# Kernel optimization log

Measured on AMD Instinct MI355X. Metric: run time of the kernel, lower is better.

The kernel has to match this reference:

```python
import jax, jax.numpy as jnp
import numpy as np

N_NODES = 50000
N_EDGES = 600000
FEAT = 128
N_LAYERS = 4


def setup_inputs() -> dict:
    key = jax.random.key(0)
    ks = jax.random.split(key, 7)
    feats = jax.random.normal(ks[0], (N_NODES, FEAT), dtype=jnp.float32)
    src = jax.random.randint(ks[1], (N_EDGES,), 0, N_NODES)
    dst = jax.random.randint(ks[2], (N_EDGES,), 0, N_NODES)
    s = 1.0 / np.sqrt(FEAT)  # torch Linear default init range
    theta_w = jax.random.uniform(ks[3], (N_LAYERS, FEAT, FEAT), jnp.float32, -s, s)
    theta_b = jax.random.uniform(ks[4], (N_LAYERS, FEAT), jnp.float32, -s, s)
    phi_w = jax.random.uniform(ks[5], (N_LAYERS, FEAT, FEAT), jnp.float32, -s, s)
    phi_b = jax.random.uniform(ks[6], (N_LAYERS, FEAT), jnp.float32, -s, s)
    return {"feats": feats, "src": src, "dst": dst,
            "theta_w": theta_w, "theta_b": theta_b,
            "phi_w": phi_w, "phi_b": phi_b}


def _edgeconv(x, src, dst, tw, tb, pw, pb):
    # EdgeConv (Wang et al. 2018): out_i = max_{(j->i) in E} theta(x_j - x_i) + phi(x_i)
    phi = x @ pw.T + pb                       # [N, F] node-level linear (avoid per-edge recompute)
    diff = x[src] - x[dst]                    # [E, F] gather
    msg = diff @ tw.T + tb + phi[dst]         # [E, F]
    agg = jax.ops.segment_max(msg, dst, num_segments=x.shape[0])  # [N, F]
    # nodes with no incoming edges get -inf from segment_max; zero them (DGL convention)
    return jnp.where(jnp.isneginf(agg), jnp.zeros_like(agg), agg)


def reference(feats, src, dst, theta_w, theta_b, phi_w, phi_b):
    x = feats
    for l in range(N_LAYERS):
        x = _edgeconv(x, src, dst, theta_w[l], theta_b[l], phi_w[l], phi_b[l])
        x = jax.nn.relu(x)
    return x
```

## Files before the change

kernel.cpp:

```cpp
#include <hip/hip_runtime.h>

#define FEAT 128

typedef __attribute__((ext_vector_type(8))) _Float16 f16x8;
typedef __attribute__((ext_vector_type(2))) _Float16 f16x2;
typedef __attribute__((ext_vector_type(4))) float f32x4;

static __device__ __forceinline__ int wave_incl_scan(int v, int lane) {
#pragma unroll
    for (int off = 1; off < 64; off <<= 1) {
        int u = __shfl_up(v, off, 64);
        if (lane >= off) v += u;
    }
    return v;
}


__global__ void hist_kernel(const int* __restrict__ dst, int* __restrict__ deg, int E) {
    int e = blockIdx.x * blockDim.x + threadIdx.x;
    if (e < E) atomicAdd(&deg[dst[e]], 1);
}

__global__ __launch_bounds__(1024) void scan1_kernel(const int* __restrict__ deg,
                                                     int* __restrict__ row_ptr,
                                                     int* __restrict__ bsum, int N) {
    int i = blockIdx.x * 1024 + threadIdx.x;
    int lane = threadIdx.x & 63;
    int w = threadIdx.x >> 6;
    int v = (i < N) ? deg[i] : 0;
    int inc = wave_incl_scan(v, lane);
    __shared__ int wsum[16];
    if (lane == 63) wsum[w] = inc;
    __syncthreads();
    if (w == 0) {
        int s = (lane < 16) ? wsum[lane] : 0;
        int si = wave_incl_scan(s, lane);
        if (lane < 16) wsum[lane] = si - s;
    }
    __syncthreads();
    int exc = inc - v + wsum[w];
    if (i < N) row_ptr[i] = exc;
    if (threadIdx.x == 1023) bsum[blockIdx.x] = exc + v;
}

__global__ __launch_bounds__(1024) void scan2_kernel(const int* __restrict__ bsum,
                                                     int* __restrict__ boff,
                                                     int* __restrict__ row_ptr,
                                                     int nb, int N, int E) {
    int tid = threadIdx.x;
    int lane = tid & 63;
    int w = tid >> 6;
    int v = (tid < nb) ? bsum[tid] : 0;
    int inc = wave_incl_scan(v, lane);
    __shared__ int wsum[16];
    if (lane == 63) wsum[w] = inc;
    __syncthreads();
    if (w == 0) {
        int s = (lane < 16) ? wsum[lane] : 0;
        int si = wave_incl_scan(s, lane);
        if (lane < 16) wsum[lane] = si - s;
    }
    __syncthreads();
    if (tid < nb) boff[tid] = inc - v + wsum[w];
    if (tid == 0) row_ptr[N] = E;
}

__global__ void scan3_kernel(int* __restrict__ row_ptr, const int* __restrict__ boff, int N) {
    int i = blockIdx.x * blockDim.x + threadIdx.x;
    if (i < N) row_ptr[i] += boff[i >> 10];
}


__global__ void wcvt_kernel(const float* __restrict__ tw, const float* __restrict__ pw,
                            const float* __restrict__ tb, const float* __restrict__ pb,
                            _Float16* __restrict__ wt, _Float16* __restrict__ wp,
                            float* __restrict__ bsum, int n, int nbias) {
    int i = blockIdx.x * blockDim.x + threadIdx.x;
    if (i < n) { wt[i] = (_Float16)tw[i]; wp[i] = (_Float16)pw[i]; }
    if (i < nbias) bsum[i] = tb[i] + pb[i];
}

__global__ void xcvt_kernel(const float* __restrict__ x, _Float16* __restrict__ x16, int n4) {
    int i = blockIdx.x * blockDim.x + threadIdx.x;
    if (i < n4) {
        float4 v = ((const float4*)x)[i];
        f16x2 a, b;
        a[0] = (_Float16)v.x; a[1] = (_Float16)v.y;
        b[0] = (_Float16)v.z; b[1] = (_Float16)v.w;
        ((f16x2*)x16)[i * 2] = a;
        ((f16x2*)x16)[i * 2 + 1] = b;
    }
}


static __device__ __forceinline__ void gemm_body(
        int bx,
        const _Float16* __restrict__ x16,
        const _Float16* __restrict__ wt, const _Float16* __restrict__ wp,
        const float* __restrict__ bias,
        _Float16* __restrict__ t16, _Float16* __restrict__ q16, int M) {
    int lane = threadIdx.x & 63;
    int l16 = lane & 15;
    int quad = lane >> 4;
    int cn0 = (threadIdx.x >> 6) * 32;

    f16x8 bt[2][4], bp[2][4];
    float biasv[2];
#pragma unroll
    for (int ct = 0; ct < 2; ++ct) {
        int col = cn0 + ct * 16 + l16;
        biasv[ct] = bias[col];
#pragma unroll
        for (int kk = 0; kk < 4; ++kk) {
            int k = kk * 32 + quad * 8;
            bt[ct][kk] = *(const f16x8*)(wt + (size_t)col * FEAT + k);
            bp[ct][kk] = *(const f16x8*)(wp + (size_t)col * FEAT + k);
        }
    }

    int rbase0 = bx * 128;
#pragma unroll 1
    for (int rs = 0; rs < 8; ++rs) {
        int rbase = rbase0 + rs * 16;
        int row = rbase + l16;
        int rowc = (row < M) ? row : (M - 1);
        f16x8 a[4];
#pragma unroll
        for (int kk = 0; kk < 4; ++kk)
            a[kk] = *(const f16x8*)(x16 + (size_t)rowc * FEAT + kk * 32 + quad * 8);

        f32x4 accT[2] = {{0.f, 0.f, 0.f, 0.f}, {0.f, 0.f, 0.f, 0.f}};
        f32x4 accP[2] = {{0.f, 0.f, 0.f, 0.f}, {0.f, 0.f, 0.f, 0.f}};
#pragma unroll
        for (int kk = 0; kk < 4; ++kk) {
#pragma unroll
            for (int ct = 0; ct < 2; ++ct) {
                accT[ct] = __builtin_amdgcn_mfma_f32_16x16x32_f16(a[kk], bt[ct][kk], accT[ct], 0, 0, 0);
                accP[ct] = __builtin_amdgcn_mfma_f32_16x16x32_f16(a[kk], bp[ct][kk], accP[ct], 0, 0, 0);
            }
        }
#pragma unroll
        for (int ct = 0; ct < 2; ++ct) {
            int col = cn0 + ct * 16 + l16;
#pragma unroll
            for (int r = 0; r < 4; ++r) {
                int ro = rbase + quad * 4 + r;
                if (ro < M) {
                    t16[(size_t)ro * FEAT + col] = (_Float16)accT[ct][r];
                    q16[(size_t)ro * FEAT + col] =
                        (_Float16)(accP[ct][r] - accT[ct][r] + biasv[ct]);
                }
            }
        }
    }
}

__global__ __launch_bounds__(256) void mfma_gemm_kernel(
        const _Float16* __restrict__ x16,
        const _Float16* __restrict__ wt, const _Float16* __restrict__ wp,
        const float* __restrict__ bias,
        _Float16* __restrict__ t16, _Float16* __restrict__ q16, int M) {
    gemm_body(blockIdx.x, x16, wt, wp, bias, t16, q16, M);
}

__global__ __launch_bounds__(256) void fused0_kernel(
        const _Float16* __restrict__ x16,
        const _Float16* __restrict__ wt, const _Float16* __restrict__ wp,
        const float* __restrict__ bias,
        _Float16* __restrict__ t16, _Float16* __restrict__ q16, int M, int gb,
        const int* __restrict__ src, const int* __restrict__ dst,
        const int* __restrict__ row_ptr, int* __restrict__ fill,
        int* __restrict__ esrc, int E) {
    if ((int)blockIdx.x < gb) {
        gemm_body(blockIdx.x, x16, wt, wp, bias, t16, q16, M);
    } else {
        int e = (blockIdx.x - gb) * 256 + threadIdx.x;
        if (e < E) {
            int d = dst[e];
            int pos = row_ptr[d] + atomicAdd(&fill[d], 1);
            esrc[pos] = src[e];
        }
    }
}


static __device__ __forceinline__ f16x8 vmax8(f16x8 a, f16x8 b) {
#pragma unroll
    for (int i = 0; i < 8; ++i) a[i] = (a[i] > b[i]) ? a[i] : b[i];
    return a;
}

static __device__ __forceinline__ f16x8 shflxor8(f16x8 v, int mask) {
    union { f16x8 h; int i[4]; } u;
    u.h = v;
#pragma unroll
    for (int k = 0; k < 4; ++k) u.i[k] = __shfl_xor(u.i[k], mask, 64);
    return u.h;
}

__global__ __launch_bounds__(256) void agg_kernel(
        const _Float16* __restrict__ t16, const _Float16* __restrict__ q16,
        const int* __restrict__ row_ptr, const int* __restrict__ esrc,
        float* __restrict__ outf, _Float16* __restrict__ ox, int N) {
    int wv = threadIdx.x >> 6;
    int lane = threadIdx.x & 63;
    int node = blockIdx.x * 4 + wv;
    if (node >= N) return;

    int g = lane >> 4;
    int c = lane & 15;

    int beg = row_ptr[node];
    int end = row_ptr[node + 1];

    if (beg >= end) {
        if (outf && g == 0) {
            float4 z = make_float4(0.f, 0.f, 0.f, 0.f);
            ((float4*)(outf + (size_t)node * FEAT + c * 8))[0] = z;
            ((float4*)(outf + (size_t)node * FEAT + c * 8))[1] = z;
        }
        if (ox && g == 0) {
            f16x8 z = {};
            *(f16x8*)(ox + (size_t)node * FEAT + c * 8) = z;
        }
        return;
    }

    const _Float16 NEGINF = (_Float16)(-65504.0f);
    f16x8 m0, m1, m2, m3;
#pragma unroll
    for (int i = 0; i < 8; ++i) { m0[i] = NEGINF; m1[i] = NEGINF; m2[i] = NEGINF; m3[i] = NEGINF; }

    for (int base = beg; base < end; base += 64) {
        int n = end - base;
        if (n > 64) n = 64;
        int nm1 = n - 1;
        int li = (lane < n) ? lane : nm1;
        int myidx = esrc[base + li];
        for (int j = 0; j < n; j += 16) {
            bool b1 = (j + 4) < n, b2 = (j + 8) < n, b3 = (j + 12) < n;
            int s0 = j + g;       if (s0 > nm1) s0 = nm1;
            f16x8 v0 = *(const f16x8*)(t16 + (size_t)__shfl(myidx, s0) * FEAT + c * 8);
            f16x8 v1, v2, v3;
            if (b1) {
                int s1 = j + 4 + g;  if (s1 > nm1) s1 = nm1;
                v1 = *(const f16x8*)(t16 + (size_t)__shfl(myidx, s1) * FEAT + c * 8);
            }
            if (b2) {
                int s2 = j + 8 + g;  if (s2 > nm1) s2 = nm1;
                v2 = *(const f16x8*)(t16 + (size_t)__shfl(myidx, s2) * FEAT + c * 8);
            }
            if (b3) {
                int s3 = j + 12 + g; if (s3 > nm1) s3 = nm1;
                v3 = *(const f16x8*)(t16 + (size_t)__shfl(myidx, s3) * FEAT + c * 8);
            }
            m0 = vmax8(m0, v0);
            if (b1) m1 = vmax8(m1, v1);
            if (b2) m2 = vmax8(m2, v2);
            if (b3) m3 = vmax8(m3, v3);
        }
    }

    f16x8 m = vmax8(vmax8(m0, m1), vmax8(m2, m3));

    m = vmax8(m, shflxor8(m, 16));
    m = vmax8(m, shflxor8(m, 32));

    if (g == 0) {
        f16x8 qi = *(const f16x8*)(q16 + (size_t)node * FEAT + c * 8);
        float o[8];
#pragma unroll
        for (int i = 0; i < 8; ++i)
            o[i] = fmaxf((float)m[i] + (float)qi[i], 0.f);

        if (outf) {
            float4 o0 = make_float4(o[0], o[1], o[2], o[3]);
            float4 o1 = make_float4(o[4], o[5], o[6], o[7]);
            ((float4*)(outf + (size_t)node * FEAT + c * 8))[0] = o0;
            ((float4*)(outf + (size_t)node * FEAT + c * 8))[1] = o1;
        }
        if (ox) {
            f16x8 oh;
#pragma unroll
            for (int i = 0; i < 8; ++i) oh[i] = (_Float16)o[i];
            *(f16x8*)(ox + (size_t)node * FEAT + c * 8) = oh;
        }
    }
}


extern "C" void kernel_launch(void* const* d_in, const int* in_sizes, int n_in,
                              void* d_out, int out_size, void* d_ws, size_t ws_size,
                              hipStream_t stream) {
    const float* feats   = (const float*)d_in[0];
    const int*   src     = (const int*)d_in[1];
    const int*   dst     = (const int*)d_in[2];
    const float* theta_w = (const float*)d_in[3];
    const float* theta_b = (const float*)d_in[4];
    const float* phi_w   = (const float*)d_in[5];
    const float* phi_b   = (const float*)d_in[6];

    const int N = in_sizes[0] / FEAT;
    const int E = in_sizes[1];
    const int L = in_sizes[3] / (FEAT * FEAT);

    char* ws = (char*)d_ws;
    size_t off = 0;
    auto alloc = [&](size_t bytes) -> void* {
        void* ptr = ws + off;
        off = (off + bytes + 255) & ~(size_t)255;
        return ptr;
    };
    _Float16* t16 = (_Float16*)alloc((size_t)N * FEAT * 2);
    _Float16* q16 = (_Float16*)alloc((size_t)N * FEAT * 2);
    _Float16* x16 = (_Float16*)alloc((size_t)N * FEAT * 2);
    _Float16* wt16 = (_Float16*)alloc((size_t)L * FEAT * FEAT * 2);
    _Float16* wp16 = (_Float16*)alloc((size_t)L * FEAT * FEAT * 2);
    float* bsum_b = (float*)alloc((size_t)L * FEAT * sizeof(float));
    int* deg     = (int*)alloc((size_t)N * sizeof(int));
    int* fill    = (int*)alloc((size_t)N * sizeof(int));
    int* row_ptr = (int*)alloc((size_t)(N + 1) * sizeof(int));
    int* esrc    = (int*)alloc((size_t)E * sizeof(int));
    int* bsum    = (int*)alloc(2048 * sizeof(int));
    int* boff    = (int*)alloc(2048 * sizeof(int));
    (void)ws_size;

    hipMemsetAsync(deg, 0, (size_t)N * sizeof(int), stream);
    hipMemsetAsync(fill, 0, (size_t)N * sizeof(int), stream);

    int eb = (E + 255) / 256;
    int nb = (N + 1023) >> 10;
    hist_kernel<<<eb, 256, 0, stream>>>(dst, deg, E);
    scan1_kernel<<<nb, 1024, 0, stream>>>(deg, row_ptr, bsum, N);
    scan2_kernel<<<1, 1024, 0, stream>>>(bsum, boff, row_ptr, nb, N, E);
    scan3_kernel<<<(N + 255) / 256, 256, 0, stream>>>(row_ptr, boff, N);

    int wn = L * FEAT * FEAT;
    wcvt_kernel<<<(wn + 255) / 256, 256, 0, stream>>>(
        theta_w, phi_w, theta_b, phi_b, wt16, wp16, bsum_b, wn, L * FEAT);
    int xn4 = N * FEAT / 4;
    xcvt_kernel<<<(xn4 + 255) / 256, 256, 0, stream>>>(feats, x16, xn4);

    int gb = (N + 127) / 128;
    for (int l = 0; l < L; ++l) {
        if (l == 0) {
            fused0_kernel<<<gb + eb, 256, 0, stream>>>(
                x16, wt16, wp16, bsum_b, t16, q16, N, gb,
                src, dst, row_ptr, fill, esrc, E);
        } else {
            mfma_gemm_kernel<<<gb, 256, 0, stream>>>(
                x16,
                wt16 + (size_t)l * FEAT * FEAT,
                wp16 + (size_t)l * FEAT * FEAT,
                bsum_b + (size_t)l * FEAT,
                t16, q16, N);
        }

        bool last = (l == L - 1);
        agg_kernel<<<(N + 3) / 4, 256, 0, stream>>>(
            t16, q16,
            row_ptr, esrc,
            last ? (float*)d_out : nullptr,
            last ? nullptr : x16,
            N);
    }
}
```

Measured before the change: 338.9 us.

## Bucket CSR edges by source slab and fuse preprocessing kernels

Builds the CSR with four sub-buckets per destination node, keyed by which quarter of the node range the source falls in. Edges are therefore gathered slab by slab, so that concurrent waves touch a smaller working set of t16 and cache reuse improves. The histogram, weight conversion and feature conversion kernels are merged into one launch. The GEMM moves to 64 rows per block for more blocks, and the aggregation loop drops the early exit for empty nodes. The cost is a scan four times larger, four row-pointer reads per node, and a single max accumulator chain.

```diff
diff --git a/kernel.cpp b/kernel.cpp
--- a/kernel.cpp
+++ b/kernel.cpp
@@ -1,6 +1,7 @@
 #include <hip/hip_runtime.h>
 
 #define FEAT 128
+#define SLABS 4
 
 typedef __attribute__((ext_vector_type(8))) _Float16 f16x8;
 typedef __attribute__((ext_vector_type(2))) _Float16 f16x2;
@@ -16,18 +17,46 @@
 }
 
 
-__global__ void hist_kernel(const int* __restrict__ dst, int* __restrict__ deg, int E) {
-    int e = blockIdx.x * blockDim.x + threadIdx.x;
-    if (e < E) atomicAdd(&deg[dst[e]], 1);
-}
+__global__ void prep_kernel(const int* __restrict__ src, const int* __restrict__ dst,
+                            int* __restrict__ deg4, int E, int slab_size,
+                            const float* __restrict__ tw, const float* __restrict__ pw,
+                            const float* __restrict__ tb, const float* __restrict__ pb,
+                            _Float16* __restrict__ wt, _Float16* __restrict__ wp,
+                            float* __restrict__ bsum, int wn, int nbias,
+                            const float* __restrict__ x, _Float16* __restrict__ x16, int xn4,
+                            int hb, int wb) {
+    int bid = blockIdx.x;
+    if (bid < hb) {
+        int e = bid * 256 + threadIdx.x;
+        if (e < E) {
+            int sl = src[e] / slab_size;
+            atomicAdd(&deg4[dst[e] * SLABS + sl], 1);
+        }
+    } else if (bid < hb + wb) {
+        int i = (bid - hb) * 256 + threadIdx.x;
+        if (i < wn) { wt[i] = (_Float16)tw[i]; wp[i] = (_Float16)pw[i]; }
+        if (i < nbias) bsum[i] = tb[i] + pb[i];
+    } else {
+        int i = (bid - hb - wb) * 256 + threadIdx.x;
+        if (i < xn4) {
+            float4 v = ((const float4*)x)[i];
+            f16x2 a, b;
+            a[0] = (_Float16)v.x; a[1] = (_Float16)v.y;
+            b[0] = (_Float16)v.z; b[1] = (_Float16)v.w;
+            ((f16x2*)x16)[i * 2] = a;
+            ((f16x2*)x16)[i * 2 + 1] = b;
+        }
+    }
+}
+
 
 __global__ __launch_bounds__(1024) void scan1_kernel(const int* __restrict__ deg,
                                                      int* __restrict__ row_ptr,
-                                                     int* __restrict__ bsum, int N) {
+                                                     int* __restrict__ bsum, int N4) {
     int i = blockIdx.x * 1024 + threadIdx.x;
     int lane = threadIdx.x & 63;
     int w = threadIdx.x >> 6;
-    int v = (i < N) ? deg[i] : 0;
+    int v = (i < N4) ? deg[i] : 0;
     int inc = wave_incl_scan(v, lane);
     __shared__ int wsum[16];
     if (lane == 63) wsum[w] = inc;
@@ -39,14 +68,14 @@
     }
     __syncthreads();
     int exc = inc - v + wsum[w];
-    if (i < N) row_ptr[i] = exc;
+    if (i < N4) row_ptr[i] = exc;
     if (threadIdx.x == 1023) bsum[blockIdx.x] = exc + v;
 }
 
 __global__ __launch_bounds__(1024) void scan2_kernel(const int* __restrict__ bsum,
                                                      int* __restrict__ boff,
                                                      int* __restrict__ row_ptr,
-                                                     int nb, int N, int E) {
+                                                     int nb, int N4, int E) {
     int tid = threadIdx.x;
     int lane = tid & 63;
     int w = tid >> 6;
@@ -62,34 +91,12 @@
     }
     __syncthreads();
     if (tid < nb) boff[tid] = inc - v + wsum[w];
-    if (tid == 0) row_ptr[N] = E;
-}
-
-__global__ void scan3_kernel(int* __restrict__ row_ptr, const int* __restrict__ boff, int N) {
+    if (tid == 0) row_ptr[N4] = E;
+}
+
+__global__ void scan3_kernel(int* __restrict__ row_ptr, const int* __restrict__ boff, int N4) {
     int i = blockIdx.x * blockDim.x + threadIdx.x;
-    if (i < N) row_ptr[i] += boff[i >> 10];
-}
-
-
-__global__ void wcvt_kernel(const float* __restrict__ tw, const float* __restrict__ pw,
-                            const float* __restrict__ tb, const float* __restrict__ pb,
-                            _Float16* __restrict__ wt, _Float16* __restrict__ wp,
-                            float* __restrict__ bsum, int n, int nbias) {
-    int i = blockIdx.x * blockDim.x + threadIdx.x;
-    if (i < n) { wt[i] = (_Float16)tw[i]; wp[i] = (_Float16)pw[i]; }
-    if (i < nbias) bsum[i] = tb[i] + pb[i];
-}
-
-__global__ void xcvt_kernel(const float* __restrict__ x, _Float16* __restrict__ x16, int n4) {
-    int i = blockIdx.x * blockDim.x + threadIdx.x;
-    if (i < n4) {
-        float4 v = ((const float4*)x)[i];
-        f16x2 a, b;
-        a[0] = (_Float16)v.x; a[1] = (_Float16)v.y;
-        b[0] = (_Float16)v.z; b[1] = (_Float16)v.w;
-        ((f16x2*)x16)[i * 2] = a;
-        ((f16x2*)x16)[i * 2 + 1] = b;
-    }
+    if (i < N4) row_ptr[i] += boff[i >> 10];
 }
 
 
@@ -118,9 +125,9 @@
         }
     }
 
-    int rbase0 = bx * 128;
+    int rbase0 = bx * 64;
 #pragma unroll 1
-    for (int rs = 0; rs < 8; ++rs) {
+    for (int rs = 0; rs < 4; ++rs) {
         int rbase = rbase0 + rs * 16;
         int row = rbase + l16;
         int rowc = (row < M) ? row : (M - 1);
@@ -169,16 +176,17 @@
         const float* __restrict__ bias,
         _Float16* __restrict__ t16, _Float16* __restrict__ q16, int M, int gb,
         const int* __restrict__ src, const int* __restrict__ dst,
-        const int* __restrict__ row_ptr, int* __restrict__ fill,
-        int* __restrict__ esrc, int E) {
+        const int* __restrict__ row_ptr4, int* __restrict__ fill4,
+        int* __restrict__ esrc, int E, int slab_size) {
     if ((int)blockIdx.x < gb) {
         gemm_body(blockIdx.x, x16, wt, wp, bias, t16, q16, M);
     } else {
         int e = (blockIdx.x - gb) * 256 + threadIdx.x;
         if (e < E) {
-            int d = dst[e];
-            int pos = row_ptr[d] + atomicAdd(&fill[d], 1);
-            esrc[pos] = src[e];
+            int s = src[e];
+            int key = dst[e] * SLABS + s / slab_size;
+            int pos = row_ptr4[key] + atomicAdd(&fill4[key], 1);
+            esrc[pos] = s;
         }
     }
 }
@@ -200,7 +208,7 @@
 
 __global__ __launch_bounds__(256) void agg_kernel(
         const _Float16* __restrict__ t16, const _Float16* __restrict__ q16,
-        const int* __restrict__ row_ptr, const int* __restrict__ esrc,
+        const int* __restrict__ row_ptr4, const int* __restrict__ esrc,
         float* __restrict__ outf, _Float16* __restrict__ ox, int N) {
     int wv = threadIdx.x >> 6;
     int lane = threadIdx.x & 63;
@@ -210,58 +218,46 @@
     int g = lane >> 4;
     int c = lane & 15;
 
-    int beg = row_ptr[node];
-    int end = row_ptr[node + 1];
-
-    if (beg >= end) {
-        if (outf && g == 0) {
-            float4 z = make_float4(0.f, 0.f, 0.f, 0.f);
-            ((float4*)(outf + (size_t)node * FEAT + c * 8))[0] = z;
-            ((float4*)(outf + (size_t)node * FEAT + c * 8))[1] = z;
-        }
-        if (ox && g == 0) {
-            f16x8 z = {};
-            *(f16x8*)(ox + (size_t)node * FEAT + c * 8) = z;
-        }
-        return;
-    }
-
     const _Float16 NEGINF = (_Float16)(-65504.0f);
-    f16x8 m0, m1, m2, m3;
-#pragma unroll
-    for (int i = 0; i < 8; ++i) { m0[i] = NEGINF; m1[i] = NEGINF; m2[i] = NEGINF; m3[i] = NEGINF; }
-
-    for (int base = beg; base < end; base += 64) {
-        int n = end - base;
-        if (n > 64) n = 64;
-        int nm1 = n - 1;
-        int li = (lane < n) ? lane : nm1;
-        int myidx = esrc[base + li];
-        for (int j = 0; j < n; j += 16) {
-            bool b1 = (j + 4) < n, b2 = (j + 8) < n, b3 = (j + 12) < n;
-            int s0 = j + g;       if (s0 > nm1) s0 = nm1;
-            f16x8 v0 = *(const f16x8*)(t16 + (size_t)__shfl(myidx, s0) * FEAT + c * 8);
-            f16x8 v1, v2, v3;
-            if (b1) {
-                int s1 = j + 4 + g;  if (s1 > nm1) s1 = nm1;
-                v1 = *(const f16x8*)(t16 + (size_t)__shfl(myidx, s1) * FEAT + c * 8);
+    f16x8 m;
+#pragma unroll
+    for (int i = 0; i < 8; ++i) m[i] = NEGINF;
+
+#pragma unroll 1
+    for (int s = 0; s < SLABS; ++s) {
+        int beg = row_ptr4[4 * node + s];
+        int end = row_ptr4[4 * node + s + 1];
+        for (int base = beg; base < end; base += 64) {
+            int n = end - base;
+            if (n > 64) n = 64;
+            int nm1 = n - 1;
+            int li = (lane < n) ? lane : nm1;
+            int myidx = esrc[base + li];
+            for (int j = 0; j < n; j += 16) {
+                bool b1 = (j + 4) < n, b2 = (j + 8) < n, b3 = (j + 12) < n;
+                int s0 = j + g;       if (s0 > nm1) s0 = nm1;
+                f16x8 v0 = *(const f16x8*)(t16 + (size_t)__shfl(myidx, s0) * FEAT + c * 8);
+                f16x8 v1, v2, v3;
+                if (b1) {
+                    int s1 = j + 4 + g;  if (s1 > nm1) s1 = nm1;
+                    v1 = *(const f16x8*)(t16 + (size_t)__shfl(myidx, s1) * FEAT + c * 8);
+                }
+                if (b2) {
+                    int s2 = j + 8 + g;  if (s2 > nm1) s2 = nm1;
+                    v2 = *(const f16x8*)(t16 + (size_t)__shfl(myidx, s2) * FEAT + c * 8);
+                }
+                if (b3) {
+                    int s3 = j + 12 + g; if (s3 > nm1) s3 = nm1;
+                    v3 = *(const f16x8*)(t16 + (size_t)__shfl(myidx, s3) * FEAT + c * 8);
+                }
+                f16x8 acc = v0;
+                if (b1) acc = vmax8(acc, v1);
+                if (b2) acc = vmax8(acc, v2);
+                if (b3) acc = vmax8(acc, v3);
+                m = vmax8(m, acc);
             }
-            if (b2) {
-                int s2 = j + 8 + g;  if (s2 > nm1) s2 = nm1;
-                v2 = *(const f16x8*)(t16 + (size_t)__shfl(myidx, s2) * FEAT + c * 8);
-            }
-            if (b3) {
-                int s3 = j + 12 + g; if (s3 > nm1) s3 = nm1;
-                v3 = *(const f16x8*)(t16 + (size_t)__shfl(myidx, s3) * FEAT + c * 8);
-            }
-            m0 = vmax8(m0, v0);
-            if (b1) m1 = vmax8(m1, v1);
-            if (b2) m2 = vmax8(m2, v2);
-            if (b3) m3 = vmax8(m3, v3);
-        }
-    }
-
-    f16x8 m = vmax8(vmax8(m0, m1), vmax8(m2, m3));
+        }
+    }
 
     m = vmax8(m, shflxor8(m, 16));
     m = vmax8(m, shflxor8(m, 32));
@@ -303,6 +299,8 @@
     const int N = in_sizes[0] / FEAT;
     const int E = in_sizes[1];
     const int L = in_sizes[3] / (FEAT * FEAT);
+    const int N4 = N * SLABS;
+    const int slab_size = (N + SLABS - 1) / SLABS;
 
     char* ws = (char*)d_ws;
     size_t off = 0;
@@ -317,36 +315,38 @@
     _Float16* wt16 = (_Float16*)alloc((size_t)L * FEAT * FEAT * 2);
     _Float16* wp16 = (_Float16*)alloc((size_t)L * FEAT * FEAT * 2);
     float* bsum_b = (float*)alloc((size_t)L * FEAT * sizeof(float));
-    int* deg     = (int*)alloc((size_t)N * sizeof(int));
-    int* fill    = (int*)alloc((size_t)N * sizeof(int));
-    int* row_ptr = (int*)alloc((size_t)(N + 1) * sizeof(int));
-    int* esrc    = (int*)alloc((size_t)E * sizeof(int));
-    int* bsum    = (int*)alloc(2048 * sizeof(int));
-    int* boff    = (int*)alloc(2048 * sizeof(int));
+    int* deg4     = (int*)alloc((size_t)N4 * sizeof(int));
+    int* fill4    = (int*)alloc((size_t)N4 * sizeof(int));
+    int* row_ptr4 = (int*)alloc((size_t)(N4 + 1) * sizeof(int));
+    int* esrc     = (int*)alloc((size_t)E * sizeof(int));
+    int* bsum     = (int*)alloc(2048 * sizeof(int));
+    int* boff     = (int*)alloc(2048 * sizeof(int));
     (void)ws_size;
 
-    hipMemsetAsync(deg, 0, (size_t)N * sizeof(int), stream);
-    hipMemsetAsync(fill, 0, (size_t)N * sizeof(int), stream);
+    hipMemsetAsync(deg4, 0, (size_t)N4 * sizeof(int), stream);
+    hipMemsetAsync(fill4, 0, (size_t)N4 * sizeof(int), stream);
 
     int eb = (E + 255) / 256;
-    int nb = (N + 1023) >> 10;
-    hist_kernel<<<eb, 256, 0, stream>>>(dst, deg, E);
-    scan1_kernel<<<nb, 1024, 0, stream>>>(deg, row_ptr, bsum, N);
-    scan2_kernel<<<1, 1024, 0, stream>>>(bsum, boff, row_ptr, nb, N, E);
-    scan3_kernel<<<(N + 255) / 256, 256, 0, stream>>>(row_ptr, boff, N);
-
     int wn = L * FEAT * FEAT;
-    wcvt_kernel<<<(wn + 255) / 256, 256, 0, stream>>>(
-        theta_w, phi_w, theta_b, phi_b, wt16, wp16, bsum_b, wn, L * FEAT);
+    int wb = (wn + 255) / 256;
     int xn4 = N * FEAT / 4;
-    xcvt_kernel<<<(xn4 + 255) / 256, 256, 0, stream>>>(feats, x16, xn4);
-
-    int gb = (N + 127) / 128;
+    int xb = (xn4 + 255) / 256;
+    prep_kernel<<<eb + wb + xb, 256, 0, stream>>>(
+        src, dst, deg4, E, slab_size,
+        theta_w, phi_w, theta_b, phi_b, wt16, wp16, bsum_b, wn, L * FEAT,
+        feats, x16, xn4, eb, wb);
+
+    int nb = (N4 + 1023) >> 10;
+    scan1_kernel<<<nb, 1024, 0, stream>>>(deg4, row_ptr4, bsum, N4);
+    scan2_kernel<<<1, 1024, 0, stream>>>(bsum, boff, row_ptr4, nb, N4, E);
+    scan3_kernel<<<(N4 + 255) / 256, 256, 0, stream>>>(row_ptr4, boff, N4);
+
+    int gb = (N + 63) / 64;
     for (int l = 0; l < L; ++l) {
         if (l == 0) {
             fused0_kernel<<<gb + eb, 256, 0, stream>>>(
                 x16, wt16, wp16, bsum_b, t16, q16, N, gb,
-                src, dst, row_ptr, fill, esrc, E);
+                src, dst, row_ptr4, fill4, esrc, E, slab_size);
         } else {
             mfma_gemm_kernel<<<gb, 256, 0, stream>>>(
                 x16,
@@ -359,7 +359,7 @@
         bool last = (l == L - 1);
         agg_kernel<<<(N + 3) / 4, 256, 0, stream>>>(
             t16, q16,
-            row_ptr, esrc,
+            row_ptr4, esrc,
             last ? (float*)d_out : nullptr,
             last ? nullptr : x16,
             N);
```

After: 403.6 us. 1.19x slower.
